# Performance work log

Measured on AMD Instinct MI355X. Metric: run time of the kernel, lower is better.

Reference implementation:

```python
import jax, jax.numpy as jnp
import numpy as np

MARGIN = 4.0  # radians, per module default margin=4 used in math.cos/math.sin
EPS = 1e-12   # matches torch F.normalize default eps


def setup_inputs() -> dict:
    key = jax.random.key(0)
    k1, k2, k3 = jax.random.split(key, 3)
    N, E, C = 4096, 512, 50257
    x = jax.random.normal(k1, (N, E), dtype=jnp.float32)
    label = jax.random.randint(k2, (N,), 0, C, dtype=jnp.int64)
    # xavier_uniform-ish init for weight [C, E]
    limit = float(np.sqrt(6.0 / (C + E)))
    weight = jax.random.uniform(k3, (C, E), dtype=jnp.float32, minval=-limit, maxval=limit)
    return {"x": x, "label": label, "weight": weight}


def reference(x, label, weight):
    N = x.shape[0]
    # L2 normalize rows (F.normalize p=2 dim=1)
    nx = x / jnp.maximum(jnp.linalg.norm(x, axis=1, keepdims=True), EPS)
    nw = weight / jnp.maximum(jnp.linalg.norm(weight, axis=1, keepdims=True), EPS)
    # cosine similarity [N, C]
    cos = jnp.einsum('ne,ce->nc', nx, nw)
    rows = jnp.arange(N)
    target = cos[rows, label]                      # [N]
    sin_t = jnp.sqrt(1.0 - target * target)
    cos_m = target * jnp.cos(MARGIN) - sin_t * jnp.sin(MARGIN)
    # replace target-class logit with margin-adjusted value
    logits = cos.at[rows, label].set(cos_m)
    # cross entropy with mean reduction
    logz = jax.nn.logsumexp(logits, axis=1)
    loss = jnp.mean(logz - logits[rows, label])
    return loss
```

## Files before the change

### kernel.cpp

```cpp
#include <hip/hip_runtime.h>
#include <math.h>

#define N_ROWS 4096
#define E_DIM  512
#define C_CLS  50257
#define NCH    786
#define NGRP   16
#define COS_M  (-0.6536436208636119f)
#define SIN_M  (-0.7568024953079282f)
#define EPSN   1e-12f

typedef __bf16 bf16x8 __attribute__((ext_vector_type(8)));
typedef float  f32x4  __attribute__((ext_vector_type(4)));
typedef unsigned short ushort8 __attribute__((ext_vector_type(8)));

__device__ inline unsigned short f2bf(float f) {
  unsigned int u = __float_as_uint(f);
  u += 0x7FFFu + ((u >> 16) & 1u);
  return (unsigned short)(u >> 16);
}
__device__ inline float bf2f(unsigned short u) {
  return __uint_as_float((unsigned)u << 16);
}

__global__ __launch_bounds__(256) void k_norm_w(const float* __restrict__ src,
                                                unsigned short* __restrict__ dst) {
  int row = blockIdx.x * 4 + (threadIdx.x >> 6);
  if (row >= C_CLS) return;
  int lane = threadIdx.x & 63;
  const float4* p = (const float4*)(src + (size_t)row * E_DIM);
  float4 v0 = p[lane * 2], v1 = p[lane * 2 + 1];
  float ss = v0.x*v0.x + v0.y*v0.y + v0.z*v0.z + v0.w*v0.w
           + v1.x*v1.x + v1.y*v1.y + v1.z*v1.z + v1.w*v1.w;
  #pragma unroll
  for (int m = 32; m > 0; m >>= 1) ss += __shfl_xor(ss, m, 64);
  float inv = 1.0f / fmaxf(sqrtf(ss), EPSN);
  ushort8 o;
  o[0]=f2bf(v0.x*inv); o[1]=f2bf(v0.y*inv); o[2]=f2bf(v0.z*inv); o[3]=f2bf(v0.w*inv);
  o[4]=f2bf(v1.x*inv); o[5]=f2bf(v1.y*inv); o[6]=f2bf(v1.z*inv); o[7]=f2bf(v1.w*inv);
  *(ushort8*)(dst + (size_t)row * E_DIM + lane * 8) = o;
}

__global__ __launch_bounds__(256) void k_norm_x(const float* __restrict__ x,
                                                const float* __restrict__ w,
                                                const int* __restrict__ label,
                                                unsigned short* __restrict__ nx,
                                                float* __restrict__ tv,
                                                float* __restrict__ tb) {
  int row = blockIdx.x;
  int lab = label[row];
  int tid = threadIdx.x;
  const float2* px = (const float2*)(x + (size_t)row * E_DIM);
  const float2* pw = (const float2*)(w + (size_t)lab * E_DIM);
  float2 a = px[tid], b = pw[tid];
  float sx = a.x*a.x + a.y*a.y;
  float sw = b.x*b.x + b.y*b.y;
  float sd = a.x*b.x + a.y*b.y;
  #pragma unroll
  for (int off = 32; off > 0; off >>= 1) {
    sx += __shfl_down(sx, off, 64);
    sw += __shfl_down(sw, off, 64);
    sd += __shfl_down(sd, off, 64);
  }
  __shared__ float sb[3][4];
  __shared__ float sb2[4];
  if ((tid & 63) == 0) {
    sb[0][tid >> 6] = sx; sb[1][tid >> 6] = sw; sb[2][tid >> 6] = sd;
  }
  __syncthreads();
  float SX = sb[0][0] + sb[0][1] + sb[0][2] + sb[0][3];
  float SW = sb[1][0] + sb[1][1] + sb[1][2] + sb[1][3];
  float invx = 1.0f / fmaxf(sqrtf(SX), EPSN);
  float invw = 1.0f / fmaxf(sqrtf(SW), EPSN);
  ushort2 o;
  o.x = f2bf(a.x * invx);
  o.y = f2bf(a.y * invx);
  ((ushort2*)(nx + (size_t)row * E_DIM))[tid] = o;
  float s2 = bf2f(o.x) * bf2f(f2bf(b.x * invw))
           + bf2f(o.y) * bf2f(f2bf(b.y * invw));
  #pragma unroll
  for (int off = 32; off > 0; off >>= 1) s2 += __shfl_down(s2, off, 64);
  if ((tid & 63) == 0) sb2[tid >> 6] = s2;
  __syncthreads();
  if (tid == 0) {
    float SD = sb[2][0] + sb[2][1] + sb[2][2] + sb[2][3];
    tv[row] = SD / (fmaxf(sqrtf(SX), EPSN) * fmaxf(sqrtf(SW), EPSN));
    tb[row] = sb2[0] + sb2[1] + sb2[2] + sb2[3];
  }
}

#define GLDS(gp, lp) __builtin_amdgcn_global_load_lds( \
    (const __attribute__((address_space(1))) void*)(gp), \
    (__attribute__((address_space(3))) void*)(lp), 16, 0, 0)

__global__ __launch_bounds__(512, 2) void k_gemm(const unsigned short* __restrict__ nx,
                                                 const unsigned short* __restrict__ nw,
                                                 float* __restrict__ pl) {
  __shared__ unsigned char ldsB[2][65536];

  const int rtile = blockIdx.x;
  const int grp   = blockIdx.y;
  const int c0    = grp * 49 + (grp < 2 ? grp : 2);
  const int c1    = c0 + 49 + (grp < 2 ? 1 : 0);

  const int tid  = threadIdx.x;
  const int wave = tid >> 6;
  const int lane = tid & 63;
  const int q    = lane >> 4;
  const int l15  = lane & 15;
  const int row0 = rtile * 256 + wave * 32;

  auto stageB = [&](int c, int p) {
    unsigned cb = (unsigned)c * 64u;
    #pragma unroll
    for (int i = 0; i < 8; i++) {
      int ch = wave * 8 + i;
      unsigned col = cb + (unsigned)(((ch >> 4) << 4) + l15);
      if (col >= C_CLS) col = C_CLS - 1;
      unsigned off = col * (unsigned)E_DIM + (unsigned)((ch & 15) * 32 + q * 8);
      GLDS(nw + off, &ldsB[p][ch * 1024]);
    }
  };

  stageB(c0, c0 & 1);

  f32x4 araw[2][16];
  #pragma unroll
  for (int rf = 0; rf < 2; rf++)
    #pragma unroll
    for (int kf = 0; kf < 16; kf++) {
      const unsigned short* pa = nx + (size_t)(row0 + rf * 16 + l15) * E_DIM
                                    + kf * 32 + q * 8;
      asm volatile("global_load_dwordx4 %0, %1, off"
                   : "=v"(araw[rf][kf]) : "v"(pa));
    }
  asm volatile("s_waitcnt vmcnt(0)" ::: "memory");
  bf16x8 a[2][16];
  #pragma unroll
  for (int rf = 0; rf < 2; rf++)
    #pragma unroll
    for (int kf = 0; kf < 16; kf++)
      a[rf][kf] = __builtin_bit_cast(bf16x8, araw[rf][kf]);

  float e[8] = {};

  __syncthreads();

  for (int c = c0; c < c1; ++c) {
    const int p = c & 1;
    if (c + 1 < c1) stageB(c + 1, p ^ 1);

    f32x4 acc[2][4] = {};
    const unsigned char* bb = &ldsB[p][0];
    #pragma unroll
    for (int ks = 0; ks < 16; ks++) {
      bf16x8 bfr[4];
      #pragma unroll
      for (int cf = 0; cf < 4; cf++)
        bfr[cf] = *(const bf16x8*)(bb + (unsigned)((cf * 16 + ks) * 1024) + (unsigned)lane * 16u);
      #pragma unroll
      for (int rf = 0; rf < 2; rf++)
        #pragma unroll
        for (int cf = 0; cf < 4; cf++)
          acc[rf][cf] = __builtin_amdgcn_mfma_f32_16x16x32_bf16(
              a[rf][ks], bfr[cf], acc[rf][cf], 0, 0, 0);
    }

    if (c != NCH - 1) {
      #pragma unroll
      for (int rf = 0; rf < 2; rf++)
        #pragma unroll
        for (int r = 0; r < 4; r++)
          #pragma unroll
          for (int cf = 0; cf < 4; cf++)
            e[rf * 4 + r] += __expf(acc[rf][cf][r]);
    } else {
      const int ccol = c * 64;
      #pragma unroll
      for (int rf = 0; rf < 2; rf++)
        #pragma unroll
        for (int r = 0; r < 4; r++)
          #pragma unroll
          for (int cf = 0; cf < 4; cf++) {
            int col = ccol + cf * 16 + l15;
            if (col < C_CLS) e[rf * 4 + r] += __expf(acc[rf][cf][r]);
          }
    }

    __syncthreads();
  }

  #pragma unroll
  for (int i = 0; i < 8; i++) {
    float s = e[i];
    #pragma unroll
    for (int m = 1; m < 16; m <<= 1) s += __shfl_xor(s, m, 64);
    if (l15 == 0) {
      int grow = row0 + (i >> 2) * 16 + 4 * q + (i & 3);
      pl[(size_t)grow * NGRP + grp] = s;
    }
  }
}

__global__ __launch_bounds__(256) void k_reduce(const float* __restrict__ pl,
                                               const float* __restrict__ tv,
                                               const float* __restrict__ tb,
                                               float* __restrict__ out) {
  int row = blockIdx.x * 256 + threadIdx.x;
  const float4* p = (const float4*)(pl + (size_t)row * NGRP);
  float4 s0 = p[0], s1 = p[1], s2 = p[2], s3 = p[3];
  float S = (s0.x + s0.y + s0.z + s0.w) + (s1.x + s1.y + s1.z + s1.w)
          + (s2.x + s2.y + s2.z + s2.w) + (s3.x + s3.y + s3.z + s3.w);
  float t = tv[row];
  float tbl = tb[row];
  float sint = sqrtf(fmaxf(0.f, 1.f - t * t));
  float cosm = t * COS_M - sint * SIN_M;
  float Sp = S - __expf(tbl) + __expf(cosm);
  float loss = logf(Sp) - cosm;
  #pragma unroll
  for (int m = 32; m > 0; m >>= 1) loss += __shfl_xor(loss, m, 64);
  if ((threadIdx.x & 63) == 0) atomicAdd(out, loss * (1.0f / N_ROWS));
}

extern "C" void kernel_launch(void* const* d_in, const int* in_sizes, int n_in,
                              void* d_out, int out_size, void* d_ws, size_t ws_size,
                              hipStream_t stream) {
  const float* x = (const float*)d_in[0];
  const int* label = (const int*)d_in[1];
  const float* w = (const float*)d_in[2];
  float* out = (float*)d_out;
  char* ws = (char*)d_ws;

  size_t off = 0;
  unsigned short* nx = (unsigned short*)(ws + off); off += (size_t)N_ROWS * E_DIM * 2;
  unsigned short* nw = (unsigned short*)(ws + off); off += (size_t)C_CLS * E_DIM * 2;
  float* tv  = (float*)(ws + off); off += (size_t)N_ROWS * 4;
  float* tb  = (float*)(ws + off); off += (size_t)N_ROWS * 4;
  float* pl  = (float*)(ws + off); off += (size_t)N_ROWS * NGRP * 4;

  hipMemsetAsync(d_out, 0, sizeof(float), stream);
  k_norm_w<<<(C_CLS + 3) / 4, 256, 0, stream>>>(w, nw);
  k_norm_x<<<N_ROWS, 256, 0, stream>>>(x, w, label, nx, tv, tb);
  dim3 g(16, 16);
  k_gemm<<<g, 512, 0, stream>>>(nx, nw, pl);
  k_reduce<<<N_ROWS / 256, 256, 0, stream>>>(pl, tv, tb, out);
}
```

Baseline: 341.3 us.

## Load last B column fragment directly from global and merge norm kernels

The GEMM now stages only three of the four 16-column B fragments per chunk into LDS and has each lane load the fourth fragment straight from global memory into registers, prefetched one k-step ahead. This shrinks the LDS buffer and the LDS read traffic, which may help occupancy and ease LDS bandwidth pressure, at the cost of extra uncoalesced-ish global loads on the critical path. The two normalization kernels are also merged into one launch to remove a kernel boundary.

```diff
diff --git a/kernel.cpp b/kernel.cpp
--- a/kernel.cpp
+++ b/kernel.cpp
@@ -23,30 +23,30 @@
   return __uint_as_float((unsigned)u << 16);
 }
 
-__global__ __launch_bounds__(256) void k_norm_w(const float* __restrict__ src,
-                                                unsigned short* __restrict__ dst) {
-  int row = blockIdx.x * 4 + (threadIdx.x >> 6);
-  if (row >= C_CLS) return;
-  int lane = threadIdx.x & 63;
-  const float4* p = (const float4*)(src + (size_t)row * E_DIM);
-  float4 v0 = p[lane * 2], v1 = p[lane * 2 + 1];
-  float ss = v0.x*v0.x + v0.y*v0.y + v0.z*v0.z + v0.w*v0.w
-           + v1.x*v1.x + v1.y*v1.y + v1.z*v1.z + v1.w*v1.w;
-  #pragma unroll
-  for (int m = 32; m > 0; m >>= 1) ss += __shfl_xor(ss, m, 64);
-  float inv = 1.0f / fmaxf(sqrtf(ss), EPSN);
-  ushort8 o;
-  o[0]=f2bf(v0.x*inv); o[1]=f2bf(v0.y*inv); o[2]=f2bf(v0.z*inv); o[3]=f2bf(v0.w*inv);
-  o[4]=f2bf(v1.x*inv); o[5]=f2bf(v1.y*inv); o[6]=f2bf(v1.z*inv); o[7]=f2bf(v1.w*inv);
-  *(ushort8*)(dst + (size_t)row * E_DIM + lane * 8) = o;
-}
-
-__global__ __launch_bounds__(256) void k_norm_x(const float* __restrict__ x,
-                                                const float* __restrict__ w,
-                                                const int* __restrict__ label,
-                                                unsigned short* __restrict__ nx,
-                                                float* __restrict__ tv,
-                                                float* __restrict__ tb) {
+__global__ __launch_bounds__(256) void k_norm(const float* __restrict__ x,
+                                              const float* __restrict__ w,
+                                              const int* __restrict__ label,
+                                              unsigned short* __restrict__ nx,
+                                              unsigned short* __restrict__ nw,
+                                              float* __restrict__ tv,
+                                              float* __restrict__ tb) {
+  if (blockIdx.x >= N_ROWS) {
+    int row = (blockIdx.x - N_ROWS) * 4 + (threadIdx.x >> 6);
+    if (row >= C_CLS) return;
+    int lane = threadIdx.x & 63;
+    const float4* p = (const float4*)(w + (size_t)row * E_DIM);
+    float4 v0 = p[lane * 2], v1 = p[lane * 2 + 1];
+    float ss = v0.x*v0.x + v0.y*v0.y + v0.z*v0.z + v0.w*v0.w
+             + v1.x*v1.x + v1.y*v1.y + v1.z*v1.z + v1.w*v1.w;
+    #pragma unroll
+    for (int m = 32; m > 0; m >>= 1) ss += __shfl_xor(ss, m, 64);
+    float inv = 1.0f / fmaxf(sqrtf(ss), EPSN);
+    ushort8 o;
+    o[0]=f2bf(v0.x*inv); o[1]=f2bf(v0.y*inv); o[2]=f2bf(v0.z*inv); o[3]=f2bf(v0.w*inv);
+    o[4]=f2bf(v1.x*inv); o[5]=f2bf(v1.y*inv); o[6]=f2bf(v1.z*inv); o[7]=f2bf(v1.w*inv);
+    *(ushort8*)(nw + (size_t)row * E_DIM + lane * 8) = o;
+    return;
+  }
   int row = blockIdx.x;
   int lab = label[row];
   int tid = threadIdx.x;
@@ -96,7 +96,7 @@
 __global__ __launch_bounds__(512, 2) void k_gemm(const unsigned short* __restrict__ nx,
                                                  const unsigned short* __restrict__ nw,
                                                  float* __restrict__ pl) {
-  __shared__ unsigned char ldsB[2][65536];
+  __shared__ unsigned char ldsB[2][49152];
 
   const int rtile = blockIdx.x;
   const int grp   = blockIdx.y;
@@ -113,13 +113,18 @@
   auto stageB = [&](int c, int p) {
     unsigned cb = (unsigned)c * 64u;
     #pragma unroll
-    for (int i = 0; i < 8; i++) {
-      int ch = wave * 8 + i;
-      unsigned col = cb + (unsigned)(((ch >> 4) << 4) + l15);
+    for (int i = 0; i < 6; i++) {
+      int ch = wave * 6 + i;
+      unsigned col = cb + (unsigned)((ch >> 4) * 16 + l15);
       if (col >= C_CLS) col = C_CLS - 1;
       unsigned off = col * (unsigned)E_DIM + (unsigned)((ch & 15) * 32 + q * 8);
       GLDS(nw + off, &ldsB[p][ch * 1024]);
     }
+  };
+  auto dirbase = [&](int c) -> const unsigned short* {
+    unsigned col = (unsigned)c * 64u + 48u + (unsigned)l15;
+    if (col >= C_CLS) col = C_CLS - 1;
+    return nw + (size_t)col * E_DIM + q * 8;
   };
 
   stageB(c0, c0 & 1);
@@ -144,27 +149,40 @@
 
   float e[8] = {};
 
+  const unsigned short* b3 = dirbase(c0);
+  bf16x8 dA = *(const bf16x8*)(b3);
+
   __syncthreads();
 
   for (int c = c0; c < c1; ++c) {
     const int p = c & 1;
     if (c + 1 < c1) stageB(c + 1, p ^ 1);
+    const unsigned short* b3n = (c + 1 < c1) ? dirbase(c + 1) : b3;
 
     f32x4 acc[2][4] = {};
     const unsigned char* bb = &ldsB[p][0];
     #pragma unroll
     for (int ks = 0; ks < 16; ks++) {
-      bf16x8 bfr[4];
-      #pragma unroll
-      for (int cf = 0; cf < 4; cf++)
-        bfr[cf] = *(const bf16x8*)(bb + (unsigned)((cf * 16 + ks) * 1024) + (unsigned)lane * 16u);
-      #pragma unroll
-      for (int rf = 0; rf < 2; rf++)
+      bf16x8 dN;
+      if (ks < 15) dN = *(const bf16x8*)(b3 + (ks + 1) * 32);
+      else         dN = *(const bf16x8*)(b3n);
+      bf16x8 bfr[3];
+      #pragma unroll
+      for (int cf = 0; cf < 3; cf++)
+        bfr[cf] = *(const bf16x8*)(bb + (unsigned)((cf * 16 + ks) * 1024)
+                                      + (unsigned)lane * 16u);
+      #pragma unroll
+      for (int rf = 0; rf < 2; rf++) {
         #pragma unroll
-        for (int cf = 0; cf < 4; cf++)
+        for (int cf = 0; cf < 3; cf++)
           acc[rf][cf] = __builtin_amdgcn_mfma_f32_16x16x32_bf16(
               a[rf][ks], bfr[cf], acc[rf][cf], 0, 0, 0);
-    }
+        acc[rf][3] = __builtin_amdgcn_mfma_f32_16x16x32_bf16(
+            a[rf][ks], dA, acc[rf][3], 0, 0, 0);
+      }
+      dA = dN;
+    }
+    b3 = b3n;
 
     if (c != NCH - 1) {
       #pragma unroll
@@ -239,8 +257,8 @@
   float* pl  = (float*)(ws + off); off += (size_t)N_ROWS * NGRP * 4;
 
   hipMemsetAsync(d_out, 0, sizeof(float), stream);
-  k_norm_w<<<(C_CLS + 3) / 4, 256, 0, stream>>>(w, nw);
-  k_norm_x<<<N_ROWS, 256, 0, stream>>>(x, w, label, nx, tv, tb);
+  int nwBlocks = (C_CLS + 3) / 4;
+  k_norm<<<N_ROWS + nwBlocks, 256, 0, stream>>>(x, w, label, nx, nw, tv, tb);
   dim3 g(16, 16);
   k_gemm<<<g, 512, 0, stream>>>(nx, nw, pl);
   k_reduce<<<N_ROWS / 256, 256, 0, stream>>>(pl, tv, tb, out);
```

Result: slower. 451.0 us (+32.1%).
